# Optimization experiments

Hardware: AMD Instinct MI355X
Metric: run time of the kernel (lower is better)

Reference implementation:

```python
import jax, jax.numpy as jnp
import numpy as np

T = 10
EPS = 1e-05

def setup_inputs() -> dict:
    key = jax.random.key(0)
    k1, k2 = jax.random.split(key)
    B, C, H, W = 128, 64, 56, 56
    X = jax.random.normal(k1, (B, C, H, W), dtype=jnp.float32)
    beta = jnp.zeros((C,), dtype=jnp.float32)
    return {"X": X, "beta": beta}


def reference(X, beta):
    # Training-path of BWItnBlock.forward (grad enabled branch of iter_norm_batch)
    B, C, H, W = X.shape
    d = C                      # n_channels, num_groups g = 1
    m = B * H * W
    # x = X.transpose(0,1).view(g, d, -1)  -> [d, m] with g=1
    x = jnp.transpose(X, (1, 0, 2, 3)).reshape(d, m)
    mean = jnp.mean(x, axis=1, keepdims=True)          # [d, 1]
    xc = x - mean                                      # [d, m]
    I = jnp.eye(d, dtype=X.dtype)
    # Sigma = eps*I + xc xc^T / m
    Sigma = EPS * I + (xc @ xc.T) / m                  # [d, d]
    # fix_cov: multiply off-diagonal by 0.9, diagonal by 1.0
    fix = 0.9 + 0.1 * I
    Sigma = Sigma * fix
    rTr = 1.0 / jnp.trace(Sigma)                       # scalar (sum(Sigma * I))
    Sigma_N = Sigma * rTr
    # Newton-Schulz iterations for inverse sqrt: P <- 1.5 P - 0.5 P^3 Sigma_N
    P = I
    for _ in range(T):
        P = 1.5 * P - 0.5 * ((P @ P @ P) @ Sigma_N)
    wm = P * jnp.sqrt(rTr)                             # whitening matrix [d, d]
    xn = wm @ xc                                       # [d, m]
    X_hat = jnp.transpose(xn.reshape(C, B, H, W), (1, 0, 2, 3))
    X_hat = X_hat + beta.reshape(1, C, 1, 1)
    return X_hat
```

## Files before the change

### kernel.cpp

```cpp
#include <hip/hip_runtime.h>
#include <hip/hip_bf16.h>

#define CH 64
#define HW 3136
#define MTOT 401408

__global__ __launch_bounds__(256) void k1_cov(const float* __restrict__ X,
                                              float* __restrict__ SR){
  __shared__ __align__(16) float tile[112*64];
  __shared__ __align__(16) float outbuf[4096];
  const int t = threadIdx.x;
  const int blk = blockIdx.x;
  const float* Xb = X + (size_t)(blk >> 2)*(CH*HW) + (blk & 3)*784;
  const int tid = t & 31, ti = tid >> 2, tj = tid & 3, ps = t >> 5;

  int cc[7], pp[7];
#pragma unroll
  for (int k=0;k<7;++k){ int f4 = k*256 + t; cc[k] = f4/28; pp[k] = f4 - cc[k]*28; }

  float acc[8][16];
#pragma unroll
  for (int i=0;i<8;++i)
#pragma unroll
    for (int j=0;j<16;++j) acc[i][j] = 0.f;
  float sums[7] = {0.f,0.f,0.f,0.f,0.f,0.f,0.f};

  for (int tl=0; tl<7; ++tl){
    const float* src = Xb + tl*112;
    __syncthreads();
#pragma unroll
    for (int k=0;k<7;++k){
      const float4 v = *(const float4*)(src + (size_t)cc[k]*HW + 4*pp[k]);
      sums[k] += (v.x + v.y) + (v.z + v.w);
      const int s = pp[k] & 15;
      const int colp = (((cc[k] >> 2) ^ s) << 2) | (cc[k] & 3);
      const int p = 4*pp[k];
      tile[(p+0)*64 + colp] = v.x;
      tile[(p+1)*64 + colp] = v.y;
      tile[(p+2)*64 + colp] = v.z;
      tile[(p+3)*64 + colp] = v.w;
    }
    __syncthreads();
    for (int pi=0; pi<14; ++pi){
      const int p = ps*14 + pi;
      const float* row = &tile[p*64];
      const int s = (p >> 2) & 15;
      const float4 va = *(const float4*)(row + (((2*ti+0) ^ s) << 2));
      const float4 vb = *(const float4*)(row + (((2*ti+1) ^ s) << 2));
      const float4 w0 = *(const float4*)(row + (((4*tj+0) ^ s) << 2));
      const float4 w1 = *(const float4*)(row + (((4*tj+1) ^ s) << 2));
      const float4 w2 = *(const float4*)(row + (((4*tj+2) ^ s) << 2));
      const float4 w3 = *(const float4*)(row + (((4*tj+3) ^ s) << 2));
      const float v[8]  = {va.x,va.y,va.z,va.w, vb.x,vb.y,vb.z,vb.w};
      const float wv[16] = {w0.x,w0.y,w0.z,w0.w, w1.x,w1.y,w1.z,w1.w,
                            w2.x,w2.y,w2.z,w2.w, w3.x,w3.y,w3.z,w3.w};
#pragma unroll
      for (int i=0;i<8;++i)
#pragma unroll
        for (int j=0;j<16;++j) acc[i][j] += v[i]*wv[j];
    }
  }
  __syncthreads();
  float* csP = tile;
#pragma unroll
  for (int k=0;k<7;++k) csP[t*8 + k] = sums[k];
  for (int w=0; w<8; ++w){
    if (ps == w){
      if (w == 0){
#pragma unroll
        for (int i=0;i<8;++i)
#pragma unroll
          for (int j=0;j<16;++j) outbuf[(8*ti+i)*64 + 16*tj + j] = acc[i][j];
      } else {
#pragma unroll
        for (int i=0;i<8;++i)
#pragma unroll
          for (int j=0;j<16;++j) outbuf[(8*ti+i)*64 + 16*tj + j] += acc[i][j];
      }
    }
    __syncthreads();
  }
#pragma unroll
  for (int k=0;k<16;++k) unsafeAtomicAdd(&SR[t + 256*k], outbuf[t + 256*k]);
  if (t < 64){
    float s = 0.f;
#pragma unroll
    for (int j=0;j<28;++j){
      const int f4 = 28*t + j;
      s += csP[(f4 & 255)*8 + (f4 >> 8)];
    }
    unsafeAtomicAdd(&SR[4096 + t], s);
  }
}

__device__ __forceinline__ void mm_AtB(const float* a, const float* b, float* out,
                                       float alpha, const float* aff, float beta_){
  const int t = threadIdx.x;
  const int c2 = 2*(t & 31);
  const int r0 = 8*(t >> 5);
  float acc[8][2];
#pragma unroll
  for (int i=0;i<8;++i){ acc[i][0]=0.f; acc[i][1]=0.f; }
  for (int k=0;k<64;++k){
    const float2 bv = *(const float2*)&b[k*64 + c2];
    const float4 a0 = *(const float4*)&a[k*64 + r0];
    const float4 a1 = *(const float4*)&a[k*64 + r0 + 4];
    const float av[8] = {a0.x,a0.y,a0.z,a0.w, a1.x,a1.y,a1.z,a1.w};
#pragma unroll
    for (int i=0;i<8;++i){ acc[i][0] += av[i]*bv.x; acc[i][1] += av[i]*bv.y; }
  }
  float res[8][2];
#pragma unroll
  for (int i=0;i<8;++i){
    float f0 = alpha*acc[i][0], f1 = alpha*acc[i][1];
    if (aff){ f0 += beta_*aff[(r0+i)*64 + c2]; f1 += beta_*aff[(r0+i)*64 + c2 + 1]; }
    res[i][0]=f0; res[i][1]=f1;
  }
  __syncthreads();
#pragma unroll
  for (int i=0;i<8;++i){
    float2 o2; o2.x = res[i][0]; o2.y = res[i][1];
    *(float2*)&out[(r0+i)*64 + c2] = o2;
  }
  __syncthreads();
}

__global__ __launch_bounds__(256) void k2_wm(const float* __restrict__ SR,
                                             const float* __restrict__ beta,
                                             float* __restrict__ WM,
                                             float* __restrict__ OFS){
  __shared__ __align__(16) float bufE[4096];
  __shared__ __align__(16) float bufA[4096];
  __shared__ __align__(16) float bufB[4096];
  __shared__ float meanv[64];
  __shared__ float scal[2];
  const int t = threadIdx.x;
  const float inv_m = 1.f/(float)MTOT;
  if (t < 64) meanv[t] = SR[4096 + t]*inv_m;
  __syncthreads();
  for (int idx=t; idx<4096; idx+=256){
    const int r = idx >> 6, c = idx & 63;
    const float cov = SR[idx]*inv_m - meanv[r]*meanv[c];
    bufE[idx] = (r==c) ? (cov + 1e-5f - 1.f) : 0.9f*cov;
  }
  __syncthreads();
  float n2 = 0.f, tr = 0.f;
  for (int idx=t; idx<4096; idx+=256){
    const float e = bufE[idx];
    n2 += e*e;
    if ((idx >> 6) == (idx & 63)) tr += e;
  }
  bufA[t] = n2; bufB[t] = tr;
  __syncthreads();
  if (t < 64){
    bufA[t] = bufA[t]+bufA[t+64]+bufA[t+128]+bufA[t+192];
    bufB[t] = bufB[t]+bufB[t+64]+bufB[t+128]+bufB[t+192];
  }
  __syncthreads();
  if (t == 0){
    float s1=0.f, s2=0.f;
    for (int i=0;i<64;++i){ s1 += bufA[i]; s2 += bufB[i]; }
    scal[0] = s1; scal[1] = s2;
  }
  __syncthreads();
  const float frob2 = scal[0];
  const float trE   = scal[1];
  float wscale = 1.f;
  const float* wmLds;
  if (frob2 < 0.04f){
    mm_AtB(bufE, bufE, bufA, 1.f, nullptr, 0.f);
    mm_AtB(bufA, bufE, bufB, 1.f, nullptr, 0.f);
    for (int idx=t; idx<4096; idx+=256){
      const int r = idx >> 6, c = idx & 63;
      bufB[idx] = ((r==c)?1.f:0.f) - 0.5f*bufE[idx] + 0.375f*bufA[idx] - 0.3125f*bufB[idx];
    }
    mm_AtB(bufA, bufA, bufE, 1.f, nullptr, 0.f);
    for (int idx=t; idx<4096; idx+=256)
      bufB[idx] += 0.2734375f*bufE[idx];
    wmLds = bufB;
  } else {
    const float rTr = 1.f/(trE + 64.f);
    for (int idx=t; idx<4096; idx+=256){
      const int r = idx >> 6, c = idx & 63;
      bufE[idx] = (bufE[idx] + ((r==c)?1.f:0.f))*rTr;
      bufA[idx] = (r==c)?1.f:0.f;
    }
    __syncthreads();
    for (int it=0; it<10; ++it){
      mm_AtB(bufA, bufE, bufB, 1.f, nullptr, 0.f);
      mm_AtB(bufA, bufB, bufB, 1.f, nullptr, 0.f);
      mm_AtB(bufA, bufB, bufA, -0.5f, bufA, 1.5f);
    }
    wscale = sqrtf(rTr);
    wmLds = bufA;
  }
  __syncthreads();
  for (int idx=t; idx<4096; idx+=256) WM[idx] = wmLds[idx]*wscale;
  if (t < 64){
    float d = 0.f;
    for (int j=0;j<64;++j) d += wmLds[t*64 + j]*meanv[j];
    OFS[t] = beta[t] - d*wscale;
  }
}

__global__ __launch_bounds__(256) void k3_apply(const float* __restrict__ X,
                                                const float* __restrict__ WM,
                                                const float* __restrict__ OFS,
                                                float* __restrict__ out){
  __shared__ __align__(16) float tile[64*256];
  const int t = threadIdx.x;
  const int w = __builtin_amdgcn_readfirstlane((int)(t >> 6));
  const int l = t & 63;
  const int pix = blockIdx.x*256 + 4*l;
  const int b = pix / HW;
  const int hw = pix - b*HW;
  const float* Xb = X + (size_t)b*(CH*HW) + hw;
#pragma unroll
  for (int k=0;k<16;++k){
    const int c = 4*k + w;
    const float4 v = *(const float4*)(Xb + (size_t)c*HW);
    *(float4*)&tile[c*256 + 4*l] = v;
  }
  __syncthreads();
  const int c0 = 16*w;
  float acc[16][4];
#pragma unroll
  for (int i=0;i<16;++i){ acc[i][0]=0.f; acc[i][1]=0.f; acc[i][2]=0.f; acc[i][3]=0.f; }
  for (int k=0;k<64;++k){
    const float4 xv = *(const float4*)&tile[k*256 + 4*l];
#pragma unroll
    for (int i=0;i<16;++i){
      const float wv = WM[(c0+i)*64 + k];
      acc[i][0] += wv*xv.x; acc[i][1] += wv*xv.y;
      acc[i][2] += wv*xv.z; acc[i][3] += wv*xv.w;
    }
  }
  float* ob = out + (size_t)b*(CH*HW) + hw;
#pragma unroll
  for (int i=0;i<16;++i){
    const float o = OFS[c0+i];
    float4 pk;
    pk.x = acc[i][0]+o; pk.y = acc[i][1]+o;
    pk.z = acc[i][2]+o; pk.w = acc[i][3]+o;
    *(float4*)(ob + (size_t)(c0+i)*HW) = pk;
  }
}

extern "C" void kernel_launch(void* const* d_in, const int* in_sizes, int n_in,
                              void* d_out, int out_size, void* d_ws, size_t ws_size,
                              hipStream_t stream){
  const float* X    = (const float*)d_in[0];
  const float* beta = (const float*)d_in[1];
  float* out = (float*)d_out;
  float* ws  = (float*)d_ws;
  float* SR  = ws;
  float* WM  = ws + 4160;
  float* OFS = WM + 4096;
  hipMemsetAsync(SR, 0, 4160*sizeof(float), stream);
  hipLaunchKernelGGL(k1_cov,   dim3(512),  dim3(256), 0, stream, X, SR);
  hipLaunchKernelGGL(k2_wm,    dim3(1),    dim3(256), 0, stream, SR, beta, WM, OFS);
  hipLaunchKernelGGL(k3_apply, dim3(1568), dim3(256), 0, stream, X, WM, OFS, out);
}
```

Before: 267.4 us.

## Compute covariance with bf16x3 split MFMA on lower-triangular blocks

Rewrites the covariance-accumulation kernel to read X directly into registers, split each fp32 value into bf16 hi and lo parts, and accumulate X·Xᵀ with three bf16 MFMA calls per block, approximating fp32 precision. Only the 10 lower-triangular 16x16 blocks are computed, and the whitening kernel mirrors the upper blocks. The shared-memory tile transpose and the scalar FMA outer product are removed, and the grid grows to 784 blocks. The trade-off is slightly reduced precision, since the lo·lo term is dropped, plus uncoalesced-ish strided global loads.

```diff
diff --git a/kernel.cpp b/kernel.cpp
--- a/kernel.cpp
+++ b/kernel.cpp
@@ -1,96 +1,108 @@
 #include <hip/hip_runtime.h>
-#include <hip/hip_bf16.h>
 
 #define CH 64
 #define HW 3136
 #define MTOT 401408
 
+typedef __attribute__((ext_vector_type(8))) short short8;
+typedef __attribute__((ext_vector_type(4))) float f32x4;
+typedef __attribute__((ext_vector_type(4))) unsigned int u32x4;
+
+__device__ __forceinline__ void split8(const float4 a, const float4 b,
+                                       short8& hi, short8& lo, float& ssum){
+  const float f[8] = {a.x,a.y,a.z,a.w, b.x,b.y,b.z,b.w};
+  u32x4 hp, lp;
+#pragma unroll
+  for (int j=0;j<4;++j){
+    const unsigned int b0 = __float_as_uint(f[2*j]);
+    const unsigned int b1 = __float_as_uint(f[2*j+1]);
+    hp[j] = (b0 >> 16) | (b1 & 0xFFFF0000u);
+    const float h0 = __uint_as_float(b0 & 0xFFFF0000u);
+    const float h1 = __uint_as_float(b1 & 0xFFFF0000u);
+    const unsigned int l0 = __float_as_uint(f[2*j]   - h0);
+    const unsigned int l1 = __float_as_uint(f[2*j+1] - h1);
+    lp[j] = (l0 >> 16) | (l1 & 0xFFFF0000u);
+  }
+  hi = __builtin_bit_cast(short8, hp);
+  lo = __builtin_bit_cast(short8, lp);
+  ssum += ((f[0]+f[1])+(f[2]+f[3])) + ((f[4]+f[5])+(f[6]+f[7]));
+}
+
 __global__ __launch_bounds__(256) void k1_cov(const float* __restrict__ X,
                                               float* __restrict__ SR){
-  __shared__ __align__(16) float tile[112*64];
-  __shared__ __align__(16) float outbuf[4096];
-  const int t = threadIdx.x;
-  const int blk = blockIdx.x;
-  const float* Xb = X + (size_t)(blk >> 2)*(CH*HW) + (blk & 3)*784;
-  const int tid = t & 31, ti = tid >> 2, tj = tid & 3, ps = t >> 5;
-
-  int cc[7], pp[7];
-#pragma unroll
-  for (int k=0;k<7;++k){ int f4 = k*256 + t; cc[k] = f4/28; pp[k] = f4 - cc[k]*28; }
-
-  float acc[8][16];
-#pragma unroll
-  for (int i=0;i<8;++i)
-#pragma unroll
-    for (int j=0;j<16;++j) acc[i][j] = 0.f;
-  float sums[7] = {0.f,0.f,0.f,0.f,0.f,0.f,0.f};
-
-  for (int tl=0; tl<7; ++tl){
-    const float* src = Xb + tl*112;
+  constexpr int RG[10] = {0,1,1,2,2,2,3,3,3,3};
+  constexpr int CG[10] = {0,0,1,0,1,2,0,1,2,3};
+  __shared__ float red[4096];
+  __shared__ float chs[64];
+
+  const int t   = threadIdx.x;
+  const int wid = __builtin_amdgcn_readfirstlane(t >> 6);
+  const int l   = t & 63;
+  const int wg  = blockIdx.x * 4 + wid;
+  const int lrow = l & 15;
+  const int lk   = (l >> 4) * 8;
+
+  f32x4 acc[10];
+#pragma unroll
+  for (int bi=0; bi<10; ++bi) acc[bi] = (f32x4){0.f,0.f,0.f,0.f};
+  float sums[4] = {0.f,0.f,0.f,0.f};
+
+  for (int i=0; i<4; ++i){
+    const int s = wg*4 + i;
+    const int b = s / 98;
+    const int p = (s - b*98) * 32;
+    const float* base = X + (size_t)b*(CH*HW) + p + lrow*HW + lk;
+    short8 fh[4], fl[4];
+#pragma unroll
+    for (int g=0; g<4; ++g){
+      const float* pg = base + (size_t)g*16*HW;
+      const float4 v0 = *(const float4*)pg;
+      const float4 v1 = *(const float4*)(pg + 4);
+      split8(v0, v1, fh[g], fl[g], sums[g]);
+    }
+#pragma unroll
+    for (int bi=0; bi<10; ++bi){
+      acc[bi] = __builtin_amdgcn_mfma_f32_16x16x32_bf16(fh[RG[bi]], fh[CG[bi]], acc[bi], 0,0,0);
+      acc[bi] = __builtin_amdgcn_mfma_f32_16x16x32_bf16(fh[RG[bi]], fl[CG[bi]], acc[bi], 0,0,0);
+      acc[bi] = __builtin_amdgcn_mfma_f32_16x16x32_bf16(fl[RG[bi]], fh[CG[bi]], acc[bi], 0,0,0);
+    }
+  }
+
+#pragma unroll
+  for (int g=0; g<4; ++g){
+    sums[g] += __shfl_xor(sums[g], 16);
+    sums[g] += __shfl_xor(sums[g], 32);
+  }
+
+  for (int w=0; w<4; ++w){
+    if (wid == w){
+#pragma unroll
+      for (int bi=0; bi<10; ++bi){
+        const int row0 = RG[bi]*16 + 4*(l>>4);
+        const int col  = CG[bi]*16 + (l&15);
+#pragma unroll
+        for (int r=0; r<4; ++r){
+          float* d = &red[(row0+r)*64 + col];
+          if (w==0) *d = acc[bi][r]; else *d += acc[bi][r];
+        }
+      }
+      if (l < 16){
+#pragma unroll
+        for (int g=0; g<4; ++g){
+          if (w==0) chs[g*16+l] = sums[g]; else chs[g*16+l] += sums[g];
+        }
+      }
+    }
     __syncthreads();
-#pragma unroll
-    for (int k=0;k<7;++k){
-      const float4 v = *(const float4*)(src + (size_t)cc[k]*HW + 4*pp[k]);
-      sums[k] += (v.x + v.y) + (v.z + v.w);
-      const int s = pp[k] & 15;
-      const int colp = (((cc[k] >> 2) ^ s) << 2) | (cc[k] & 3);
-      const int p = 4*pp[k];
-      tile[(p+0)*64 + colp] = v.x;
-      tile[(p+1)*64 + colp] = v.y;
-      tile[(p+2)*64 + colp] = v.z;
-      tile[(p+3)*64 + colp] = v.w;
-    }
-    __syncthreads();
-    for (int pi=0; pi<14; ++pi){
-      const int p = ps*14 + pi;
-      const float* row = &tile[p*64];
-      const int s = (p >> 2) & 15;
-      const float4 va = *(const float4*)(row + (((2*ti+0) ^ s) << 2));
-      const float4 vb = *(const float4*)(row + (((2*ti+1) ^ s) << 2));
-      const float4 w0 = *(const float4*)(row + (((4*tj+0) ^ s) << 2));
-      const float4 w1 = *(const float4*)(row + (((4*tj+1) ^ s) << 2));
-      const float4 w2 = *(const float4*)(row + (((4*tj+2) ^ s) << 2));
-      const float4 w3 = *(const float4*)(row + (((4*tj+3) ^ s) << 2));
-      const float v[8]  = {va.x,va.y,va.z,va.w, vb.x,vb.y,vb.z,vb.w};
-      const float wv[16] = {w0.x,w0.y,w0.z,w0.w, w1.x,w1.y,w1.z,w1.w,
-                            w2.x,w2.y,w2.z,w2.w, w3.x,w3.y,w3.z,w3.w};
-#pragma unroll
-      for (int i=0;i<8;++i)
-#pragma unroll
-        for (int j=0;j<16;++j) acc[i][j] += v[i]*wv[j];
-    }
-  }
-  __syncthreads();
-  float* csP = tile;
-#pragma unroll
-  for (int k=0;k<7;++k) csP[t*8 + k] = sums[k];
-  for (int w=0; w<8; ++w){
-    if (ps == w){
-      if (w == 0){
-#pragma unroll
-        for (int i=0;i<8;++i)
-#pragma unroll
-          for (int j=0;j<16;++j) outbuf[(8*ti+i)*64 + 16*tj + j] = acc[i][j];
-      } else {
-#pragma unroll
-        for (int i=0;i<8;++i)
-#pragma unroll
-          for (int j=0;j<16;++j) outbuf[(8*ti+i)*64 + 16*tj + j] += acc[i][j];
-      }
-    }
-    __syncthreads();
-  }
-#pragma unroll
-  for (int k=0;k<16;++k) unsafeAtomicAdd(&SR[t + 256*k], outbuf[t + 256*k]);
-  if (t < 64){
-    float s = 0.f;
-#pragma unroll
-    for (int j=0;j<28;++j){
-      const int f4 = 28*t + j;
-      s += csP[(f4 & 255)*8 + (f4 >> 8)];
-    }
-    unsafeAtomicAdd(&SR[4096 + t], s);
-  }
+  }
+
+#pragma unroll
+  for (int bi=0; bi<10; ++bi){
+    const int r = RG[bi]*16 + (t>>4);
+    const int c = CG[bi]*16 + (t&15);
+    unsafeAtomicAdd(&SR[r*64+c], red[r*64+c]);
+  }
+  if (t < 64) unsafeAtomicAdd(&SR[4096+t], chs[t]);
 }
 
 __device__ __forceinline__ void mm_AtB(const float* a, const float* b, float* out,
@@ -140,7 +152,8 @@
   __syncthreads();
   for (int idx=t; idx<4096; idx+=256){
     const int r = idx >> 6, c = idx & 63;
-    const float cov = SR[idx]*inv_m - meanv[r]*meanv[c];
+    const int src = ((r >> 4) >= (c >> 4)) ? idx : (c*64 + r);
+    const float cov = SR[src]*inv_m - meanv[r]*meanv[c];
     bufE[idx] = (r==c) ? (cov + 1e-5f - 1.f) : 0.9f*cov;
   }
   __syncthreads();
@@ -257,7 +270,7 @@
   float* WM  = ws + 4160;
   float* OFS = WM + 4096;
   hipMemsetAsync(SR, 0, 4160*sizeof(float), stream);
-  hipLaunchKernelGGL(k1_cov,   dim3(512),  dim3(256), 0, stream, X, SR);
+  hipLaunchKernelGGL(k1_cov,   dim3(784),  dim3(256), 0, stream, X, SR);
   hipLaunchKernelGGL(k2_wm,    dim3(1),    dim3(256), 0, stream, SR, beta, WM, OFS);
   hipLaunchKernelGGL(k3_apply, dim3(1568), dim3(256), 0, stream, X, WM, OFS, out);
 }
```

Result: faster. 260.6 us (-2.5%).
